# Kernel tuning notes

Hardware: AMD Instinct MI355X
Metric: run time of the kernel (lower is better)

Reference implementation:

```python
import jax, jax.numpy as jnp
import numpy as np

DIM = 1024
NUM_HEADS = 16
HEAD_DIM = DIM // NUM_HEADS
SCALE = HEAD_DIM ** (-0.5)


def setup_inputs() -> dict:
    key = jax.random.key(0)
    ks = jax.random.split(key, 10)
    b, nq, nkv = 1, 4096, 4096
    s = DIM ** -0.5
    return {
        "q": jax.random.normal(ks[0], (b, nq, DIM), jnp.float32),
        "kv": jax.random.normal(ks[1], (b, nkv, DIM), jnp.float32),
        "q_w": jax.random.normal(ks[2], (DIM, DIM), jnp.float32) * s,
        "q_b": jnp.zeros((DIM,), jnp.float32),
        "k_w": jax.random.normal(ks[3], (DIM, DIM), jnp.float32) * s,
        "k_b": jnp.zeros((DIM,), jnp.float32),
        "v_w": jax.random.normal(ks[4], (DIM, DIM), jnp.float32) * s,
        "v_b": jnp.zeros((DIM,), jnp.float32),
        "o_w": jax.random.normal(ks[5], (DIM, DIM), jnp.float32) * s,
        "o_b": jnp.zeros((DIM,), jnp.float32),
    }


def reference(q, kv, q_w, q_b, k_w, k_b, v_w, v_b, o_w, o_b):
    b, nq, _ = q.shape
    nkv = kv.shape[1]
    h, c = NUM_HEADS, HEAD_DIM
    # projections (torch Linear: x @ W^T + b); split into heads
    qh = (q @ q_w.T + q_b).reshape(b, nq, h, c).transpose(0, 2, 1, 3)   # b h nq c
    kh = (kv @ k_w.T + k_b).reshape(b, nkv, h, c).transpose(0, 2, 1, 3)  # b h nkv c
    vh = (kv @ v_w.T + v_b).reshape(b, nkv, h, c).transpose(0, 2, 1, 3)  # b h nkv c
    # full attention score matrix (non-fused, as in source)
    attn = jnp.einsum('bhqc,bhkc->bhqk', qh, kh) * SCALE
    attn = jax.nn.softmax(attn, axis=-1)
    out = jnp.einsum('bhqk,bhkc->bhqc', attn, vh)  # b h nq c
    out = out.transpose(0, 2, 1, 3).reshape(b, nq, h * c)
    out = out @ o_w.T + o_b
    return out
```

## Files before the change

### kernel.cpp

```cpp
#include <hip/hip_runtime.h>


typedef unsigned short ushort_t;
typedef unsigned short ushort4v __attribute__((ext_vector_type(4)));
typedef unsigned short ushort8 __attribute__((ext_vector_type(8)));
typedef __bf16 bf16x8 __attribute__((ext_vector_type(8)));
typedef float f32x4 __attribute__((ext_vector_type(4)));
typedef float f32x16 __attribute__((ext_vector_type(16)));

#define SEQ 4096
#define DIM 1024
#define NH 16
#define HD 64
#define QSCALE 0.18033688011112042f

__device__ inline ushort_t fcvt(float f) {
    return __builtin_bit_cast(ushort_t, (__bf16)f);
}
__device__ inline bf16x8 frag_of(ushort8 t) {
    return __builtin_bit_cast(bf16x8, t);
}
__device__ inline bf16x8 lds_frag(const ushort_t* p) {
    return frag_of(*(const ushort8*)p);
}
__device__ inline void gload_lds16(const void* g, void* l) {
    __builtin_amdgcn_global_load_lds(
        (const __attribute__((address_space(1))) void*)g,
        (__attribute__((address_space(3))) void*)l, 16, 0, 0);
}

__global__ __launch_bounds__(256) void cvt2(
    const float* __restrict__ s0, ushort_t* __restrict__ d0,
    const float* __restrict__ s1, ushort_t* __restrict__ d1, int n8)
{
    const float* s = blockIdx.y ? s1 : s0;
    ushort_t*    d = blockIdx.y ? d1 : d0;
    int i = blockIdx.x * 256 + threadIdx.x;
    if (i >= n8) return;
    const f32x4* sp = (const f32x4*)s + (size_t)i * 2;
    f32x4 a = sp[0], b = sp[1];
    ushort8 o;
    for (int k = 0; k < 4; ++k) { o[k] = fcvt(a[k]); o[k + 4] = fcvt(b[k]); }
    *((ushort8*)d + i) = o;
}

__global__ __launch_bounds__(256) void cvt4(
    const float* __restrict__ s0, ushort_t* __restrict__ d0,
    const float* __restrict__ s1, ushort_t* __restrict__ d1,
    const float* __restrict__ s2, ushort_t* __restrict__ d2,
    const float* __restrict__ s3, ushort_t* __restrict__ d3, int n8)
{
    const float* ss[4] = {s0, s1, s2, s3};
    ushort_t*    dd[4] = {d0, d1, d2, d3};
    const float* s = ss[blockIdx.y];
    ushort_t*    d = dd[blockIdx.y];
    int i = blockIdx.x * 256 + threadIdx.x;
    if (i >= n8) return;
    const f32x4* sp = (const f32x4*)s + (size_t)i * 2;
    f32x4 a = sp[0], b = sp[1];
    ushort8 o;
    for (int k = 0; k < 4; ++k) { o[k] = fcvt(a[k]); o[k + 4] = fcvt(b[k]); }
    *((ushort8*)d + i) = o;
}

template <bool OUT_F32, bool TRANS_OUT>
__global__ __launch_bounds__(256) void gemm_bf16(
    const ushort_t* __restrict__ A, const ushort_t* __restrict__ W,
    const float* __restrict__ bias, void* __restrict__ Cv, float scale)
{
    __shared__ __align__(16) ushort_t sA[128 * 64];
    __shared__ __align__(16) ushort_t sB[64 * 64];

    const int tid  = threadIdx.x;
    const int w    = tid >> 6;
    const int lane = tid & 63;
    const int quad = lane >> 4;
    const int l15  = lane & 15;
    const int wm   = w >> 1;
    const int wn   = w & 1;
    const int m0   = blockIdx.y * 128;
    const int n0   = blockIdx.x * 64;

    f32x4 acc[4][2] = {};

    for (int kt = 0; kt < DIM; kt += 64) {
        __syncthreads();
        for (int r = 0; r < 4; ++r) {
            int c = r * 256 + tid;
            gload_lds16(A + (size_t)(m0 + (c >> 3)) * DIM + kt + ((c & 7) << 3),
                        (char*)sA + (r * 256 + (tid & ~63)) * 16);
        }
        for (int r = 0; r < 2; ++r) {
            int c = r * 256 + tid;
            gload_lds16(W + (size_t)(n0 + (c >> 3)) * DIM + kt + ((c & 7) << 3),
                        (char*)sB + (r * 256 + (tid & ~63)) * 16);
        }
        __syncthreads();

        for (int ks = 0; ks < 2; ++ks) {
            bf16x8 af[4], bf[2];
            for (int i = 0; i < 4; ++i)
                af[i] = lds_frag(sA + (wm * 64 + i * 16 + l15) * 64 + ks * 32 + quad * 8);
            for (int j = 0; j < 2; ++j)
                bf[j] = lds_frag(sB + (wn * 32 + j * 16 + l15) * 64 + ks * 32 + quad * 8);
            for (int i = 0; i < 4; ++i)
                for (int j = 0; j < 2; ++j)
                    acc[i][j] = __builtin_amdgcn_mfma_f32_16x16x32_bf16(
                        af[i], bf[j], acc[i][j], 0, 0, 0);
        }
    }

    for (int j = 0; j < 2; ++j) {
        int col = n0 + wn * 32 + j * 16 + l15;
        float bj = bias[col];
        for (int i = 0; i < 4; ++i) {
            int row = m0 + wm * 64 + i * 16 + quad * 4;
            if constexpr (TRANS_OUT) {
                ushort4v o4;
                for (int r = 0; r < 4; ++r) o4[r] = fcvt((acc[i][j][r] + bj) * scale);
                *(ushort4v*)((ushort_t*)Cv + (size_t)col * SEQ + row) = o4;
            } else if constexpr (OUT_F32) {
                for (int r = 0; r < 4; ++r)
                    ((float*)Cv)[(size_t)(row + r) * DIM + col] = acc[i][j][r] + bj;
            } else {
                for (int r = 0; r < 4; ++r)
                    ((ushort_t*)Cv)[(size_t)(row + r) * DIM + col] =
                        fcvt((acc[i][j][r] + bj) * scale);
            }
        }
    }
}

#define BUFE (2 * 64 * 72)
__global__ __launch_bounds__(256) void attn_kernel(
    const ushort_t* __restrict__ Q, const ushort_t* __restrict__ K,
    const ushort_t* __restrict__ VT, ushort_t* __restrict__ O)
{
    __shared__ __align__(16) ushort_t sB[2 * BUFE];

    const int tid  = threadIdx.x;
    const int w    = tid >> 6;
    const int lane = tid & 63;
    const int l31  = lane & 31;
    const int hi   = lane >> 5;
    const int h    = blockIdx.x;
    const int q0   = blockIdx.y * 128 + w * 32;
    const int hHD  = h * HD;

    const int srow0 = tid >> 3;
    const int srow1 = (tid + 256) >> 3;
    const int sch   = (tid & 7) << 3;
    const ushort_t* Kg0 = K  + (size_t)srow0 * DIM + hHD + sch;
    const ushort_t* Kg1 = K  + (size_t)srow1 * DIM + hHD + sch;
    const ushort_t* Vg0 = VT + (size_t)(hHD + srow0) * SEQ + sch;
    const ushort_t* Vg1 = VT + (size_t)(hHD + srow1) * SEQ + sch;
    const int l0 = srow0 * 72 + sch, l1 = srow1 * 72 + sch;

    const ushort_t* qb = Q + (size_t)(q0 + l31) * DIM + hHD + hi * 8;
    bf16x8 qf[4];
    for (int ks = 0; ks < 4; ++ks)
        qf[ks] = frag_of(*(const ushort8*)(qb + ks * 16));

    *(ushort8*)(sB + l0)        = *(const ushort8*)(Kg0);
    *(ushort8*)(sB + l1)        = *(const ushort8*)(Kg1);
    *(ushort8*)(sB + 4608 + l0) = *(const ushort8*)(Vg0);
    *(ushort8*)(sB + 4608 + l1) = *(const ushort8*)(Vg1);
    __syncthreads();

    f32x16 oacc[2] = {};
    float l_i = 0.f;

    for (int it = 0; it < SEQ / 64; ++it) {
        const int cur = it & 1;
        const int kvn = (it + 1) * 64;
        ushort_t* bK = sB + cur * BUFE;
        ushort_t* bV = bK + 4608;

        ushort8 gk0, gk1, gv0, gv1;
        if (kvn < SEQ) {
            gk0 = *(const ushort8*)(Kg0 + (size_t)kvn * DIM);
            gk1 = *(const ushort8*)(Kg1 + (size_t)kvn * DIM);
            gv0 = *(const ushort8*)(Vg0 + kvn);
            gv1 = *(const ushort8*)(Vg1 + kvn);
        }

        bf16x8 kf[8], vf[8];
        for (int t = 0; t < 2; ++t)
            for (int ks = 0; ks < 4; ++ks)
                kf[t * 4 + ks] = lds_frag(bK + (t * 32 + l31) * 72 + ks * 16 + hi * 8);
        for (int ks = 0; ks < 4; ++ks)
            for (int dt = 0; dt < 2; ++dt)
                vf[ks * 2 + dt] = lds_frag(bV + (dt * 32 + l31) * 72 + ks * 16 + hi * 8);

        f32x16 sacc[2] = {};
        for (int t = 0; t < 2; ++t)
            for (int ks = 0; ks < 4; ++ks)
                sacc[t] = __builtin_amdgcn_mfma_f32_32x32x16_bf16(
                    kf[t * 4 + ks], qf[ks], sacc[t], 0, 0, 0);

        __syncthreads();

        float lp = 0.f;
        for (int t = 0; t < 2; ++t)
            for (int r = 0; r < 16; ++r) {
                float p = __builtin_amdgcn_exp2f(sacc[t][r]);
                sacc[t][r] = p;
                lp += p;
            }
        l_i += lp + __shfl_xor(lp, 32);

        ushort_t* pw = bK + w * 2304;
        for (int t = 0; t < 2; ++t)
            for (int g = 0; g < 4; ++g) {
                ushort4v pk;
                for (int r = 0; r < 4; ++r) pk[r] = fcvt(sacc[t][g * 4 + r]);
                *(ushort4v*)(pw + l31 * 72 + t * 32 + g * 8 + hi * 4) = pk;
            }

        for (int ks = 0; ks < 4; ++ks) {
            bf16x8 pf = lds_frag(pw + l31 * 72 + ks * 16 + hi * 8);
            for (int dt = 0; dt < 2; ++dt)
                oacc[dt] = __builtin_amdgcn_mfma_f32_32x32x16_bf16(
                    vf[ks * 2 + dt], pf, oacc[dt], 0, 0, 0);
        }

        if (kvn < SEQ) {
            ushort_t* nB = sB + (cur ^ 1) * BUFE;
            *(ushort8*)(nB + l0)        = gk0;
            *(ushort8*)(nB + l1)        = gk1;
            *(ushort8*)(nB + 4608 + l0) = gv0;
            *(ushort8*)(nB + 4608 + l1) = gv1;
        }
        __syncthreads();
    }

    float inv = 1.f / l_i;
    int qrow = q0 + l31;
    for (int dt = 0; dt < 2; ++dt)
        for (int g = 0; g < 4; ++g) {
            ushort4v o4;
            for (int r = 0; r < 4; ++r) o4[r] = fcvt(oacc[dt][g * 4 + r] * inv);
            *(ushort4v*)(O + (size_t)qrow * DIM + hHD + dt * 32 + g * 8 + hi * 4) = o4;
        }
}

extern "C" void kernel_launch(void* const* d_in, const int* in_sizes, int n_in,
                              void* d_out, int out_size, void* d_ws, size_t ws_size,
                              hipStream_t stream)
{
    const float* q   = (const float*)d_in[0];
    const float* kv  = (const float*)d_in[1];
    const float* q_w = (const float*)d_in[2];
    const float* q_b = (const float*)d_in[3];
    const float* k_w = (const float*)d_in[4];
    const float* k_b = (const float*)d_in[5];
    const float* v_w = (const float*)d_in[6];
    const float* v_b = (const float*)d_in[7];
    const float* o_w = (const float*)d_in[8];
    const float* o_b = (const float*)d_in[9];
    float* out = (float*)d_out;

    const size_t SD = (size_t)SEQ * DIM;
    const size_t WW = (size_t)DIM * DIM;
    ushort_t* Qp  = (ushort_t*)d_ws;
    ushort_t* Kp  = Qp + SD;
    ushort_t* VpT = Kp + SD;
    ushort_t* AO  = VpT + SD;
    ushort_t* Qb  = AO;
    ushort_t* KVb = AO + SD;
    ushort_t* qwb = KVb + SD;
    ushort_t* kwb = qwb + WW;
    ushort_t* vwb = kwb + WW;
    ushort_t* owb = vwb + WW;

    cvt2<<<dim3((unsigned)(SD / 8 / 256), 2), 256, 0, stream>>>(
        q, Qb, kv, KVb, (int)(SD / 8));
    cvt4<<<dim3((unsigned)(WW / 8 / 256), 4), 256, 0, stream>>>(
        q_w, qwb, k_w, kwb, v_w, vwb, o_w, owb, (int)(WW / 8));

    dim3 gg(DIM / 64, SEQ / 128);
    gemm_bf16<false, false><<<gg, 256, 0, stream>>>(Qb,  qwb, q_b, Qp,  QSCALE);
    gemm_bf16<false, false><<<gg, 256, 0, stream>>>(KVb, kwb, k_b, Kp,  1.0f);
    gemm_bf16<false, true ><<<gg, 256, 0, stream>>>(KVb, vwb, v_b, VpT, 1.0f);
    attn_kernel<<<dim3(NH, SEQ / 128), 256, 0, stream>>>(Qp, Kp, VpT, AO);
    gemm_bf16<true,  false><<<gg, 256, 0, stream>>>(AO, owb, o_b, out, 1.0f);
}
```

Before: 281.3 us.

## Double-buffer GEMM LDS tiles with register prefetch and merge QKV projections

The GEMM is rewritten to use padded, double-buffered LDS tiles with a K-step of 32. The next tile is prefetched into registers while MFMAs run on the current tile. This replaces the direct global-to-LDS loads, which needed two barriers per step, and the padding is meant to cut LDS bank conflicts. The three Q/K/V projection launches are merged into one launch with a z-dimension; the trade-off is a smaller K-step and more register-staged copies.

Measured after the change: 271.6 us. -3.5%, faster.

```diff
diff --git a/kernel.cpp b/kernel.cpp
--- a/kernel.cpp
+++ b/kernel.cpp
@@ -14,6 +14,10 @@
 #define HD 64
 #define QSCALE 0.18033688011112042f
 
+#define LSTR 40
+#define ABUF (128 * LSTR)
+#define BBUF (64 * LSTR)
+
 __device__ inline ushort_t fcvt(float f) {
     return __builtin_bit_cast(ushort_t, (__bf16)f);
 }
@@ -22,11 +26,6 @@
 }
 __device__ inline bf16x8 lds_frag(const ushort_t* p) {
     return frag_of(*(const ushort8*)p);
-}
-__device__ inline void gload_lds16(const void* g, void* l) {
-    __builtin_amdgcn_global_load_lds(
-        (const __attribute__((address_space(1))) void*)g,
-        (__attribute__((address_space(3))) void*)l, 16, 0, 0);
 }
 
 __global__ __launch_bounds__(256) void cvt2(
@@ -63,70 +62,133 @@
     *((ushort8*)d + i) = o;
 }
 
-template <bool OUT_F32, bool TRANS_OUT>
-__global__ __launch_bounds__(256) void gemm_bf16(
+__device__ __attribute__((always_inline)) inline void gemm_core(
     const ushort_t* __restrict__ A, const ushort_t* __restrict__ W,
-    const float* __restrict__ bias, void* __restrict__ Cv, float scale)
-{
-    __shared__ __align__(16) ushort_t sA[128 * 64];
-    __shared__ __align__(16) ushort_t sB[64 * 64];
-
-    const int tid  = threadIdx.x;
-    const int w    = tid >> 6;
+    int m0, int n0, int tid, f32x4 (&acc)[4][2], ushort_t* sA, ushort_t* sB)
+{
     const int lane = tid & 63;
     const int quad = lane >> 4;
     const int l15  = lane & 15;
-    const int wm   = w >> 1;
-    const int wn   = w & 1;
-    const int m0   = blockIdx.y * 128;
-    const int n0   = blockIdx.x * 64;
+    const int wm   = (tid >> 6) >> 1;
+    const int wn   = (tid >> 6) & 1;
+
+    const int ar0 = tid >> 2;
+    const int ar1 = (tid + 256) >> 2;
+    const int ac  = (tid & 3) << 3;
+    const int br  = tid >> 2;
+    const ushort_t* Ag0 = A + (size_t)(m0 + ar0) * DIM + ac;
+    const ushort_t* Ag1 = A + (size_t)(m0 + ar1) * DIM + ac;
+    const ushort_t* Wg  = W + (size_t)(n0 + br) * DIM + ac;
+    const int la0 = ar0 * LSTR + ac, la1 = ar1 * LSTR + ac, lb = br * LSTR + ac;
+
+    *(ushort8*)(sA + la0) = *(const ushort8*)(Ag0);
+    *(ushort8*)(sA + la1) = *(const ushort8*)(Ag1);
+    *(ushort8*)(sB + lb)  = *(const ushort8*)(Wg);
+    __syncthreads();
+
+    for (int it = 0; it < DIM / 32; ++it) {
+        const int cur = it & 1;
+        const int ktn = (it + 1) * 32;
+        ushort_t* aC = sA + cur * ABUF;
+        ushort_t* bC = sB + cur * BBUF;
+
+        ushort8 ga0, ga1, gb0;
+        if (ktn < DIM) {
+            ga0 = *(const ushort8*)(Ag0 + ktn);
+            ga1 = *(const ushort8*)(Ag1 + ktn);
+            gb0 = *(const ushort8*)(Wg + ktn);
+        }
+
+        bf16x8 af[4], bf[2];
+        for (int i = 0; i < 4; ++i)
+            af[i] = lds_frag(aC + (wm * 64 + i * 16 + l15) * LSTR + quad * 8);
+        for (int j = 0; j < 2; ++j)
+            bf[j] = lds_frag(bC + (wn * 32 + j * 16 + l15) * LSTR + quad * 8);
+        for (int i = 0; i < 4; ++i)
+            for (int j = 0; j < 2; ++j)
+                acc[i][j] = __builtin_amdgcn_mfma_f32_16x16x32_bf16(
+                    af[i], bf[j], acc[i][j], 0, 0, 0);
+
+        if (ktn < DIM) {
+            ushort_t* aN = sA + (cur ^ 1) * ABUF;
+            ushort_t* bN = sB + (cur ^ 1) * BBUF;
+            *(ushort8*)(aN + la0) = ga0;
+            *(ushort8*)(aN + la1) = ga1;
+            *(ushort8*)(bN + lb)  = gb0;
+        }
+        __syncthreads();
+    }
+}
+
+__global__ __launch_bounds__(256) void proj3(
+    const ushort_t* __restrict__ Qb, const ushort_t* __restrict__ KVb,
+    const ushort_t* __restrict__ qwb, const ushort_t* __restrict__ kwb,
+    const ushort_t* __restrict__ vwb,
+    const float* __restrict__ q_b, const float* __restrict__ k_b,
+    const float* __restrict__ v_b,
+    ushort_t* __restrict__ Qp, ushort_t* __restrict__ Kp,
+    ushort_t* __restrict__ VpT)
+{
+    __shared__ __align__(16) ushort_t sA[2 * ABUF];
+    __shared__ __align__(16) ushort_t sB[2 * BBUF];
+
+    const int z = blockIdx.z;
+    const ushort_t* A = z ? KVb : Qb;
+    const ushort_t* W = (z == 0) ? qwb : (z == 1 ? kwb : vwb);
+    const float* bias = (z == 0) ? q_b : (z == 1 ? k_b : v_b);
+    const int tid = threadIdx.x;
+    const int m0 = blockIdx.y * 128;
+    const int n0 = blockIdx.x * 64;
 
     f32x4 acc[4][2] = {};
-
-    for (int kt = 0; kt < DIM; kt += 64) {
-        __syncthreads();
-        for (int r = 0; r < 4; ++r) {
-            int c = r * 256 + tid;
-            gload_lds16(A + (size_t)(m0 + (c >> 3)) * DIM + kt + ((c & 7) << 3),
-                        (char*)sA + (r * 256 + (tid & ~63)) * 16);
-        }
-        for (int r = 0; r < 2; ++r) {
-            int c = r * 256 + tid;
-            gload_lds16(W + (size_t)(n0 + (c >> 3)) * DIM + kt + ((c & 7) << 3),
-                        (char*)sB + (r * 256 + (tid & ~63)) * 16);
-        }
-        __syncthreads();
-
-        for (int ks = 0; ks < 2; ++ks) {
-            bf16x8 af[4], bf[2];
-            for (int i = 0; i < 4; ++i)
-                af[i] = lds_frag(sA + (wm * 64 + i * 16 + l15) * 64 + ks * 32 + quad * 8);
-            for (int j = 0; j < 2; ++j)
-                bf[j] = lds_frag(sB + (wn * 32 + j * 16 + l15) * 64 + ks * 32 + quad * 8);
-            for (int i = 0; i < 4; ++i)
-                for (int j = 0; j < 2; ++j)
-                    acc[i][j] = __builtin_amdgcn_mfma_f32_16x16x32_bf16(
-                        af[i], bf[j], acc[i][j], 0, 0, 0);
-        }
-    }
+    gemm_core(A, W, m0, n0, tid, acc, sA, sB);
+
+    const int lane = tid & 63, quad = lane >> 4, l15 = lane & 15;
+    const int wm = (tid >> 6) >> 1, wn = (tid >> 6) & 1;
+    const float scale = (z == 0) ? QSCALE : 1.0f;
 
     for (int j = 0; j < 2; ++j) {
         int col = n0 + wn * 32 + j * 16 + l15;
         float bj = bias[col];
         for (int i = 0; i < 4; ++i) {
             int row = m0 + wm * 64 + i * 16 + quad * 4;
-            if constexpr (TRANS_OUT) {
+            if (z == 2) {
                 ushort4v o4;
-                for (int r = 0; r < 4; ++r) o4[r] = fcvt((acc[i][j][r] + bj) * scale);
-                *(ushort4v*)((ushort_t*)Cv + (size_t)col * SEQ + row) = o4;
-            } else if constexpr (OUT_F32) {
+                for (int r = 0; r < 4; ++r) o4[r] = fcvt(acc[i][j][r] + bj);
+                *(ushort4v*)(VpT + (size_t)col * SEQ + row) = o4;
+            } else {
+                ushort_t* C = z ? Kp : Qp;
                 for (int r = 0; r < 4; ++r)
-                    ((float*)Cv)[(size_t)(row + r) * DIM + col] = acc[i][j][r] + bj;
-            } else {
-                for (int r = 0; r < 4; ++r)
-                    ((ushort_t*)Cv)[(size_t)(row + r) * DIM + col] =
+                    C[(size_t)(row + r) * DIM + col] =
                         fcvt((acc[i][j][r] + bj) * scale);
             }
+        }
+    }
+}
+
+__global__ __launch_bounds__(256) void gemm_out(
+    const ushort_t* __restrict__ A, const ushort_t* __restrict__ W,
+    const float* __restrict__ bias, float* __restrict__ C)
+{
+    __shared__ __align__(16) ushort_t sA[2 * ABUF];
+    __shared__ __align__(16) ushort_t sB[2 * BBUF];
+
+    const int tid = threadIdx.x;
+    const int m0 = blockIdx.y * 128;
+    const int n0 = blockIdx.x * 64;
+
+    f32x4 acc[4][2] = {};
+    gemm_core(A, W, m0, n0, tid, acc, sA, sB);
+
+    const int lane = tid & 63, quad = lane >> 4, l15 = lane & 15;
+    const int wm = (tid >> 6) >> 1, wn = (tid >> 6) & 1;
+    for (int j = 0; j < 2; ++j) {
+        int col = n0 + wn * 32 + j * 16 + l15;
+        float bj = bias[col];
+        for (int i = 0; i < 4; ++i) {
+            int row = m0 + wm * 64 + i * 16 + quad * 4;
+            for (int r = 0; r < 4; ++r)
+                C[(size_t)(row + r) * DIM + col] = acc[i][j][r] + bj;
         }
     }
 }
@@ -278,10 +340,8 @@
     cvt4<<<dim3((unsigned)(WW / 8 / 256), 4), 256, 0, stream>>>(
         q_w, qwb, k_w, kwb, v_w, vwb, o_w, owb, (int)(WW / 8));
 
-    dim3 gg(DIM / 64, SEQ / 128);
-    gemm_bf16<false, false><<<gg, 256, 0, stream>>>(Qb,  qwb, q_b, Qp,  QSCALE);
-    gemm_bf16<false, false><<<gg, 256, 0, stream>>>(KVb, kwb, k_b, Kp,  1.0f);
-    gemm_bf16<false, true ><<<gg, 256, 0, stream>>>(KVb, vwb, v_b, VpT, 1.0f);
+    proj3<<<dim3(DIM / 64, SEQ / 128, 3), 256, 0, stream>>>(
+        Qb, KVb, qwb, kwb, vwb, q_b, k_b, v_b, Qp, Kp, VpT);
     attn_kernel<<<dim3(NH, SEQ / 128), 256, 0, stream>>>(Qp, Kp, VpT, AO);
-    gemm_bf16<true,  false><<<gg, 256, 0, stream>>>(AO, owb, o_b, out, 1.0f);
-}
+    gemm_out<<<dim3(DIM / 64, SEQ / 128), 256, 0, stream>>>(AO, owb, o_b, out);
+}
```
